# Performance work log

Measured on AMD Instinct MI355X. Metric: run time of the kernel, lower is better.

The kernel has to match this reference:

```python
import jax, jax.numpy as jnp
import numpy as np

KERNEL = 5
DILATIONS = (3, 1)
N_HEADS = 8
LN_EPS = 1e-5


def unfold1d(x, kernel, dilation, pad):
    # x: (N, H, S) -> (N, H, S, kernel) dilated sliding windows (same length)
    xp = jnp.pad(x, ((0, 0), (0, 0), (pad, pad)))
    S = x.shape[-1]
    idx = jnp.arange(S)[:, None] + jnp.arange(kernel)[None, :] * dilation  # (S, K)
    return xp[:, :, idx]  # (N, H, S, K)


def dilated_mha(q, k, v, Ws, bs, Wo, bo):
    # q,k,v: (B, S, D); Ws: (2, split, split); Wo: (D, D)
    B, S, D = q.shape
    ndil = len(DILATIONS)
    hpd = N_HEADS // ndil            # heads per dilation
    dk = D // N_HEADS
    split = D // ndil
    scale = dk ** (-0.5)
    outs, probs = [], []
    for i, dil in enumerate(DILATIONS):
        pad = dil * (KERNEL - 1) // 2
        sl = slice(i * split, (i + 1) * split)
        qi = q[..., sl] @ Ws[i].T + bs[i]
        ki = k[..., sl] @ Ws[i].T + bs[i]
        vi = v[..., sl] @ Ws[i].T + bs[i]
        # (B,S,hpd,dk) -> (B,dk,hpd,S), matching torch transpose(1,2).permute(0,3,1,2)
        to4 = lambda x: jnp.transpose(x.reshape(B, S, hpd, dk), (0, 3, 2, 1))
        qi4, ki4, vi4 = to4(qi), to4(ki), to4(vi)
        # unfold then reinterpret (B*dk,hpd,...) as (B*hpd,dk,...) exactly as torch .reshape does
        kp = unfold1d(ki4.reshape(B * dk, hpd, S), KERNEL, dil, pad).reshape(B * hpd, dk, S, KERNEL)
        vp = unfold1d(vi4.reshape(B * dk, hpd, S), KERNEL, dil, pad).reshape(B * hpd, dk, S, KERNEL)
        qr = qi4.reshape(B * hpd, dk, S)
        scores = jnp.einsum('nds,ndsk->nsk', qr, kp) * scale   # (B*hpd, S, K)
        p = jax.nn.softmax(scores, axis=-1)
        out = jnp.einsum('nsk,ndsk->nds', p, vp)               # (B*hpd, dk, S)
        out = jnp.transpose(out.reshape(B, hpd, dk, S), (0, 3, 1, 2)).reshape(B, S, split)
        outs.append(out)
        probs.append(p.reshape(B, hpd, S, KERNEL))
    o = jnp.concatenate(outs, axis=-1) @ Wo.T + bo
    return o, jnp.concatenate(probs, axis=1)


def layer_norm(x, g, b):
    mu = jnp.mean(x, axis=-1, keepdims=True)
    var = jnp.mean((x - mu) ** 2, axis=-1, keepdims=True)
    return (x - mu) * jax.lax.rsqrt(var + LN_EPS) * g + b


def setup_inputs() -> dict:
    key = jax.random.key(0)
    ks = jax.random.split(key, 6)
    B, S, D = 32, 2048, 256
    split = D // 2
    q_emb = jax.random.normal(ks[0], (B, S, D), dtype=jnp.float32)
    s_emb = jax.random.normal(ks[1], (B, S, D), dtype=jnp.float32)
    lens = jax.random.randint(ks[2], (B,), 5, S, dtype=jnp.int32)
    W_lin = jax.random.normal(ks[3], (3, 2, split, split), dtype=jnp.float32) * (split ** -0.5)
    b_lin = jnp.zeros((3, 2, split), dtype=jnp.float32)
    W_out = jax.random.normal(ks[4], (3, D, D), dtype=jnp.float32) * (D ** -0.5)
    b_out = jnp.zeros((3, D), dtype=jnp.float32)
    ln_g = jnp.ones((3, D), dtype=jnp.float32)
    ln_b = jnp.zeros((3, D), dtype=jnp.float32)
    return {"q_emb": q_emb, "s_emb": s_emb, "lens": lens, "W_lin": W_lin,
            "b_lin": b_lin, "W_out": W_out, "b_out": b_out, "ln_g": ln_g, "ln_b": ln_b}


def reference(q_emb, s_emb, lens, W_lin, b_lin, W_out, b_out, ln_g, ln_b):
    # CASTransformer.forward, shortcut=True path, eval mode (dropout=id, mask unused)
    a1, _ = dilated_mha(q_emb, q_emb, q_emb, W_lin[0], b_lin[0], W_out[0], b_out[0])
    hq = layer_norm(q_emb + a1, ln_g[0], ln_b[0])
    a2, q_scores = dilated_mha(s_emb, s_emb, s_emb, W_lin[1], b_lin[1], W_out[1], b_out[1])
    hs = layer_norm(s_emb + a2, ln_g[1], ln_b[1])
    a3, _ = dilated_mha(hq, hq, hs, W_lin[2], b_lin[2], W_out[2], b_out[2])
    z = layer_norm(hq + a3, ln_g[2], ln_b[2])
    return z, q_scores
```

## Files before the change

### kernel.cpp

```cpp
#include <hip/hip_runtime.h>
#include <hip/hip_bf16.h>

typedef __bf16 bf16x8 __attribute__((ext_vector_type(8)));
typedef float  f32x4  __attribute__((ext_vector_type(4)));
typedef unsigned int u32;
typedef u32 u32x4 __attribute__((ext_vector_type(4)));
typedef unsigned short ushort_t;

__device__ inline float bf2f(ushort_t h) {
    union { u32 u; float f; } v; v.u = ((u32)h) << 16; return v.f;
}
__device__ inline ushort_t f2bf(float f) {
    union { float f; u32 u; } v; v.f = f;
    u32 u = v.u;
    return (ushort_t)((u + 0x7fffu + ((u >> 16) & 1u)) >> 16);
}
__device__ inline bf16x8 load_bf8(const ushort_t* p) {
    u32x4 u = *reinterpret_cast<const u32x4*>(p);
    return __builtin_bit_cast(bf16x8, u);
}
__device__ inline bf16x8 load8_in(const void* base, size_t idx, int f32flag) {
    if (!f32flag) return load_bf8((const ushort_t*)base + idx);
    const float* pf = (const float*)base + idx;
    f32x4 a = *reinterpret_cast<const f32x4*>(pf);
    f32x4 b = *reinterpret_cast<const f32x4*>(pf + 4);
    bf16x8 r;
#pragma unroll
    for (int j = 0; j < 4; ++j) { r[j] = (__bf16)a[j]; r[4 + j] = (__bf16)b[j]; }
    return r;
}
__device__ inline float ld_in(const void* base, size_t idx, int f32flag) {
    return f32flag ? ((const float*)base)[idx] : bf2f(((const ushort_t*)base)[idx]);
}

#define XT_STRIDE 264

__global__ __launch_bounds__(256) void detect_kernel(const u32* __restrict__ d, int n,
                                                     int* __restrict__ flag) {
    const int t = threadIdx.x;
    int cn = 0, co = 0;
    for (int i = t; i < n; i += 256) {
        const u32 w = d[i];
        const u32 e  = (w >> 7) & 0xFF;
        const u32 fe = (w >> 23) & 0xFF;
        cn += (e >= 100 && e <= 135) ? 1 : 0;
        co += (((w & 0xFFFFu) == 0u) && fe >= 100 && fe <= 140) ? 1 : 0;
    }
    __shared__ int sn[256], so[256];
    sn[t] = cn; so[t] = co; __syncthreads();
    for (int o = 128; o; o >>= 1) {
        if (t < o) { sn[t] += sn[t + o]; so[t] += so[t + o]; }
        __syncthreads();
    }
    if (t == 0) {
        const int CN = sn[0], CO = so[0];
        const int is_f32 = (2 * CN < n) && ((2 * CO > n) || (20 * CN > n));
        *flag = is_f32 ? 1 : 0;
    }
}

__device__ inline int f_of(const int* flags, int i) { return i < 0 ? 0 : flags[i]; }
__device__ inline int out_f32(const int* flags) {
    return flags[0] | flags[1] | flags[3] | flags[4] | flags[5] | flags[6] | flags[7] | flags[8];
}

__global__ __launch_bounds__(256) void proj_kernel(
    const void* __restrict__ X, int xi,
    const void* __restrict__ W, size_t lw,
    const void* __restrict__ Bv, size_t lb,
    ushort_t* __restrict__ Y, const int* __restrict__ flags)
{
    const int xf = f_of(flags, xi);
    const int wf = flags[3], bf = flags[4];
    const int tid  = threadIdx.x;
    const int wave = tid >> 6, lane = tid & 63;
    const int dil  = wave >> 1;
    const int n_off = (wave & 1) * 64;
    const int m0   = blockIdx.x * 64;
    const int l15  = lane & 15, quad = lane >> 4;

    f32x4 acc[4][4] = {};
    for (int kc = 0; kc < 4; ++kc) {
        bf16x8 a[4], b[4];
#pragma unroll
        for (int mt = 0; mt < 4; ++mt)
            a[mt] = load8_in(X, (size_t)(m0 + mt * 16 + l15) * 256 + dil * 128 + kc * 32 + quad * 8, xf);
#pragma unroll
        for (int nt = 0; nt < 4; ++nt)
            b[nt] = load8_in(W, lw + (size_t)dil * 16384 + (size_t)(n_off + nt * 16 + l15) * 128 + kc * 32 + quad * 8, wf);
#pragma unroll
        for (int mt = 0; mt < 4; ++mt)
#pragma unroll
            for (int nt = 0; nt < 4; ++nt)
                acc[mt][nt] = __builtin_amdgcn_mfma_f32_16x16x32_bf16(a[mt], b[nt], acc[mt][nt], 0, 0, 0);
    }
#pragma unroll
    for (int mt = 0; mt < 4; ++mt) {
#pragma unroll
        for (int nt = 0; nt < 4; ++nt) {
            const int ncol = n_off + nt * 16 + l15;
            const float bias = ld_in(Bv, lb + dil * 128 + ncol, bf);
#pragma unroll
            for (int r = 0; r < 4; ++r) {
                const int row = m0 + mt * 16 + quad * 4 + r;
                Y[(size_t)row * 256 + dil * 128 + ncol] = f2bf(acc[mt][nt][r] + bias);
            }
        }
    }
}

__global__ __launch_bounds__(256) void proj_inplace_kernel(
    ushort_t* __restrict__ X,
    const void* __restrict__ W, size_t lw,
    const void* __restrict__ Bv, size_t lb,
    const int* __restrict__ flags)
{
    __shared__ ushort_t xt[64 * XT_STRIDE];
    const int wf = flags[3], bf = flags[4];
    const int tid = threadIdx.x;
    const int m0  = blockIdx.x * 64;
#pragma unroll
    for (int i = 0; i < 8; ++i) {
        const int chunk = tid + 256 * i;
        const int row = chunk >> 5, cc = chunk & 31;
        *reinterpret_cast<u32x4*>(&xt[row * XT_STRIDE + cc * 8]) =
            *reinterpret_cast<const u32x4*>(X + (size_t)(m0 + row) * 256 + cc * 8);
    }
    __syncthreads();

    const int wave = tid >> 6, lane = tid & 63;
    const int dil  = wave >> 1;
    const int n_off = (wave & 1) * 64;
    const int l15  = lane & 15, quad = lane >> 4;

    f32x4 acc[4][4] = {};
    for (int kc = 0; kc < 4; ++kc) {
        bf16x8 a[4], b[4];
#pragma unroll
        for (int mt = 0; mt < 4; ++mt)
            a[mt] = load_bf8(&xt[(mt * 16 + l15) * XT_STRIDE + dil * 128 + kc * 32 + quad * 8]);
#pragma unroll
        for (int nt = 0; nt < 4; ++nt)
            b[nt] = load8_in(W, lw + (size_t)dil * 16384 + (size_t)(n_off + nt * 16 + l15) * 128 + kc * 32 + quad * 8, wf);
#pragma unroll
        for (int mt = 0; mt < 4; ++mt)
#pragma unroll
            for (int nt = 0; nt < 4; ++nt)
                acc[mt][nt] = __builtin_amdgcn_mfma_f32_16x16x32_bf16(a[mt], b[nt], acc[mt][nt], 0, 0, 0);
    }
#pragma unroll
    for (int mt = 0; mt < 4; ++mt) {
#pragma unroll
        for (int nt = 0; nt < 4; ++nt) {
            const int ncol = n_off + nt * 16 + l15;
            const float bias = ld_in(Bv, lb + dil * 128 + ncol, bf);
#pragma unroll
            for (int r = 0; r < 4; ++r) {
                const int row = m0 + mt * 16 + quad * 4 + r;
                X[(size_t)row * 256 + dil * 128 + ncol] = f2bf(acc[mt][nt][r] + bias);
            }
        }
    }
}

__global__ __launch_bounds__(256) void fused_attn_oln_kernel(
    const ushort_t* __restrict__ P, const ushort_t* __restrict__ V,
    const void* __restrict__ R, int ri,
    const void* __restrict__ W, size_t lw,
    const void* __restrict__ Bv, size_t lb,
    const void* __restrict__ G, const void* __restrict__ Bt, size_t lg,
    void* __restrict__ H, int h_out,
    void* __restrict__ probs_base,
    const int* __restrict__ flags)
{
    __shared__ ushort_t xt[64 * XT_STRIDE];
    __shared__ float lsum[4][64], lsq[4][64];

    const int wf = flags[5], bvf = flags[6], gf = flags[7], btf = flags[8];
    const int rf = f_of(flags, ri);
    const int og = out_f32(flags);
    const int of = h_out ? og : 0;

    const int tid = threadIdx.x;
    const int m0  = blockIdx.x * 64;
    const int bb  = m0 >> 11;
    const int s0  = m0 & 2047;
    const size_t rowbase = (size_t)bb * 2048;
    const float scale = 0.17677669529663687f;

#pragma unroll
    for (int it = 0; it < 2; ++it) {
        const int task = tid + 256 * it;
        const int r  = task & 63;
        const int dg = task >> 6;
        const int dil = dg >> 2, g = dg & 3;
        const int dila = dil ? 1 : 3;
        const int s = s0 + r;
        const size_t chan0 = (size_t)dil * 128 + g * 8;

        const ushort_t* qr = P + (rowbase + s) * 256 + chan0;
        float qv[4][8];
#pragma unroll
        for (int h = 0; h < 4; ++h) {
            bf16x8 t = load_bf8(qr + h * 32);
#pragma unroll
            for (int j = 0; j < 8; ++j) qv[h][j] = (float)t[j];
        }
        float sc[5];
#pragma unroll
        for (int kk = 0; kk < 5; ++kk) {
            const int sp = s + (kk - 2) * dila;
            float a = 0.f;
            if (sp >= 0 && sp < 2048) {
                const ushort_t* kr = P + (rowbase + sp) * 256 + chan0;
#pragma unroll
                for (int h = 0; h < 4; ++h) {
                    bf16x8 t = load_bf8(kr + h * 32);
#pragma unroll
                    for (int j = 0; j < 8; ++j) a += qv[h][j] * (float)t[j];
                }
                a *= scale;
            }
            sc[kk] = a;
        }
        float mx = sc[0];
#pragma unroll
        for (int kk = 1; kk < 5; ++kk) mx = fmaxf(mx, sc[kk]);
        float p[5], sum = 0.f;
#pragma unroll
        for (int kk = 0; kk < 5; ++kk) { p[kk] = __expf(sc[kk] - mx); sum += p[kk]; }
        const float inv = 1.f / sum;
#pragma unroll
        for (int kk = 0; kk < 5; ++kk) p[kk] *= inv;

        float o[4][8] = {};
#pragma unroll
        for (int kk = 0; kk < 5; ++kk) {
            const int sp = s + (kk - 2) * dila;
            if (sp < 0 || sp >= 2048) continue;
            const ushort_t* vr = V + (rowbase + sp) * 256 + chan0;
#pragma unroll
            for (int h = 0; h < 4; ++h) {
                bf16x8 t = load_bf8(vr + h * 32);
#pragma unroll
                for (int j = 0; j < 8; ++j) o[h][j] += p[kk] * (float)t[j];
            }
        }
        ushort_t* op = &xt[r * XT_STRIDE + dil * 128 + g * 32];
#pragma unroll
        for (int c = 0; c < 4; ++c) {
            u32x4 w;
#pragma unroll
            for (int t4 = 0; t4 < 4; ++t4) {
                const int d2a = c * 8 + t4 * 2, d2b = d2a + 1;
                const u32 lo = f2bf(o[d2a & 3][d2a >> 2]);
                const u32 hi = f2bf(o[d2b & 3][d2b >> 2]);
                w[t4] = lo | (hi << 16);
            }
            *reinterpret_cast<u32x4*>(op + c * 8) = w;
        }
        if (probs_base != nullptr) {
            const size_t pb = 16777216 + ((size_t)((bb * 8 + dg) * 2048 + s)) * 5;
            if (og) {
                float* pp = (float*)probs_base;
#pragma unroll
                for (int kk = 0; kk < 5; ++kk) pp[pb + kk] = p[kk];
            } else {
                ushort_t* pp = (ushort_t*)probs_base;
#pragma unroll
                for (int kk = 0; kk < 5; ++kk) pp[pb + kk] = f2bf(p[kk]);
            }
        }
    }
    __syncthreads();

    const int wave = tid >> 6, lane = tid & 63;
    const int n_off = wave * 64;
    const int l15 = lane & 15, quad = lane >> 4;

    f32x4 acc[4][4] = {};
    for (int kc = 0; kc < 8; ++kc) {
        bf16x8 a[4], b[4];
#pragma unroll
        for (int mt = 0; mt < 4; ++mt)
            a[mt] = load_bf8(&xt[(mt * 16 + l15) * XT_STRIDE + kc * 32 + quad * 8]);
#pragma unroll
        for (int nt = 0; nt < 4; ++nt)
            b[nt] = load8_in(W, lw + (size_t)(n_off + nt * 16 + l15) * 256 + kc * 32 + quad * 8, wf);
#pragma unroll
        for (int mt = 0; mt < 4; ++mt)
#pragma unroll
            for (int nt = 0; nt < 4; ++nt)
                acc[mt][nt] = __builtin_amdgcn_mfma_f32_16x16x32_bf16(a[mt], b[nt], acc[mt][nt], 0, 0, 0);
    }

    float bias[4];
#pragma unroll
    for (int nt = 0; nt < 4; ++nt) bias[nt] = ld_in(Bv, lb + n_off + nt * 16 + l15, bvf);

    float psum[4][4] = {}, psq[4][4] = {};
#pragma unroll
    for (int mt = 0; mt < 4; ++mt) {
#pragma unroll
        for (int rr = 0; rr < 4; ++rr) {
            const size_t rrow = (size_t)(m0 + mt * 16 + quad * 4 + rr) * 256 + l15;
#pragma unroll
            for (int nt = 0; nt < 4; ++nt) {
                float v = acc[mt][nt][rr] + bias[nt] + ld_in(R, rrow + n_off + nt * 16, rf);
                acc[mt][nt][rr] = v;
                psum[mt][rr] += v;
                psq[mt][rr]  += v * v;
            }
        }
    }
#pragma unroll
    for (int off = 1; off <= 8; off <<= 1) {
#pragma unroll
        for (int mt = 0; mt < 4; ++mt)
#pragma unroll
            for (int rr = 0; rr < 4; ++rr) {
                psum[mt][rr] += __shfl_xor(psum[mt][rr], off);
                psq[mt][rr]  += __shfl_xor(psq[mt][rr],  off);
            }
    }
    if (l15 == 0) {
#pragma unroll
        for (int mt = 0; mt < 4; ++mt)
#pragma unroll
            for (int rr = 0; rr < 4; ++rr) {
                const int row = mt * 16 + quad * 4 + rr;
                lsum[wave][row] = psum[mt][rr];
                lsq[wave][row]  = psq[mt][rr];
            }
    }
    __syncthreads();

    float gl[4], bl[4];
#pragma unroll
    for (int nt = 0; nt < 4; ++nt) {
        gl[nt] = ld_in(G,  lg + n_off + nt * 16 + l15, gf);
        bl[nt] = ld_in(Bt, lg + n_off + nt * 16 + l15, btf);
    }
#pragma unroll
    for (int mt = 0; mt < 4; ++mt) {
#pragma unroll
        for (int rr = 0; rr < 4; ++rr) {
            const int row = mt * 16 + quad * 4 + rr;
            const float sm = lsum[0][row] + lsum[1][row] + lsum[2][row] + lsum[3][row];
            const float q2 = lsq[0][row]  + lsq[1][row]  + lsq[2][row]  + lsq[3][row];
            const float mu  = sm * (1.f / 256.f);
            const float var = q2 * (1.f / 256.f) - mu * mu;
            const float rs  = rsqrtf(var + 1e-5f);
            const size_t hrow = (size_t)(m0 + row) * 256 + l15;
#pragma unroll
            for (int nt = 0; nt < 4; ++nt) {
                const float hv = (acc[mt][nt][rr] - mu) * rs * gl[nt] + bl[nt];
                if (of) ((float*)H)[hrow + n_off + nt * 16] = hv;
                else    ((ushort_t*)H)[hrow + n_off + nt * 16] = f2bf(hv);
            }
        }
    }
}

extern "C" void kernel_launch(void* const* d_in, const int* in_sizes, int n_in,
                              void* d_out, int out_size, void* d_ws, size_t ws_size,
                              hipStream_t stream) {
    const void* q_emb = d_in[0];
    const void* s_emb = d_in[1];
    const void* W_lin = d_in[3];
    const void* b_lin = d_in[4];
    const void* W_out = d_in[5];
    const void* b_out = d_in[6];
    const void* ln_g  = d_in[7];
    const void* ln_b  = d_in[8];

    const size_t SLOT = 16777216;
    int*      flags = (int*)d_ws;
    ushort_t* SA = (ushort_t*)((char*)d_ws + 256);
    ushort_t* SB = SA + SLOT;
    ushort_t* SC = SA + 2 * SLOT;

    const dim3 blk(256);
    detect_kernel<<<1, blk, 0, stream>>>((const u32*)q_emb, 16384, flags + 0);
    detect_kernel<<<1, blk, 0, stream>>>((const u32*)s_emb, 16384, flags + 1);
    detect_kernel<<<1, blk, 0, stream>>>((const u32*)W_lin, 16384, flags + 3);
    detect_kernel<<<1, blk, 0, stream>>>((const u32*)b_lin,   384, flags + 4);
    detect_kernel<<<1, blk, 0, stream>>>((const u32*)W_out, 16384, flags + 5);
    detect_kernel<<<1, blk, 0, stream>>>((const u32*)b_out,   384, flags + 6);
    detect_kernel<<<1, blk, 0, stream>>>((const u32*)ln_g,    384, flags + 7);
    detect_kernel<<<1, blk, 0, stream>>>((const u32*)ln_b,    384, flags + 8);

    proj_kernel<<<1024, blk, 0, stream>>>(q_emb, 0, W_lin, 0, b_lin, 0, SC, flags);
    fused_attn_oln_kernel<<<1024, blk, 0, stream>>>(SC, SC, q_emb, 0,
        W_out, 0, b_out, 0, ln_g, ln_b, 0, SA, 0, nullptr, flags);
    proj_kernel<<<1024, blk, 0, stream>>>(s_emb, 1, W_lin, 32768, b_lin, 256, SC, flags);
    fused_attn_oln_kernel<<<1024, blk, 0, stream>>>(SC, SC, s_emb, 1,
        W_out, 65536, b_out, 256, ln_g, ln_b, 256, SB, 0, d_out, flags);
    proj_kernel<<<1024, blk, 0, stream>>>(SA, -1, W_lin, 65536, b_lin, 512, SC, flags);
    proj_inplace_kernel<<<1024, blk, 0, stream>>>(SB, W_lin, 65536, b_lin, 512, flags);
    fused_attn_oln_kernel<<<1024, blk, 0, stream>>>(SC, SB, SA, -1,
        W_out, 131072, b_out, 512, ln_g, ln_b, 512, d_out, 1, nullptr, flags);
}
```

Baseline: 697.8 us.

## Fuse input projections and next-stage projections into per-stage mega kernels

Merges the eight detect launches into one multi-block kernel. Folds each stage's QKV projection into the attention kernel: projected rows for the block plus an 8-row halo on each side go into LDS, so attention reads from shared memory rather than a global intermediate. The LayerNorm output is also projected right away with the third-stage weights, which removes the separate proj and in-place proj launches. This cuts launches and global round trips for intermediates, at the cost of recomputing the halo rows, more LDS per block (possible occupancy loss), and weights held in registers.

```diff
diff --git a/kernel.cpp b/kernel.cpp
--- a/kernel.cpp
+++ b/kernel.cpp
@@ -33,14 +33,35 @@
     return f32flag ? ((const float*)base)[idx] : bf2f(((const ushort_t*)base)[idx]);
 }
 
-#define XT_STRIDE 264
-
-__global__ __launch_bounds__(256) void detect_kernel(const u32* __restrict__ d, int n,
-                                                     int* __restrict__ flag) {
+__device__ inline int f_of(const int* flags, int i) { return i < 0 ? 0 : flags[i]; }
+__device__ inline int out_f32(const int* flags) {
+    return flags[0] | flags[1] | flags[3] | flags[4] | flags[5] | flags[6] | flags[7] | flags[8];
+}
+
+#define PT_ROWS   80
+#define PT_STRIDE 266
+#define XT_STRIDE 266
+
+__global__ __launch_bounds__(256) void detect8_kernel(
+    const u32* p0, int n0, const u32* p1, int n1, const u32* p2, int n2, const u32* p3, int n3,
+    const u32* p4, int n4, const u32* p5, int n5, const u32* p6, int n6, const u32* p7, int n7,
+    int* __restrict__ flags)
+{
+    const u32* p; int n, slot;
+    switch (blockIdx.x) {
+        case 0: p = p0; n = n0; slot = 0; break;
+        case 1: p = p1; n = n1; slot = 1; break;
+        case 2: p = p2; n = n2; slot = 3; break;
+        case 3: p = p3; n = n3; slot = 4; break;
+        case 4: p = p4; n = n4; slot = 5; break;
+        case 5: p = p5; n = n5; slot = 6; break;
+        case 6: p = p6; n = n6; slot = 7; break;
+        default: p = p7; n = n7; slot = 8; break;
+    }
     const int t = threadIdx.x;
     int cn = 0, co = 0;
     for (int i = t; i < n; i += 256) {
-        const u32 w = d[i];
+        const u32 w = p[i];
         const u32 e  = (w >> 7) & 0xFF;
         const u32 fe = (w >> 23) & 0xFF;
         cn += (e >= 100 && e <= 135) ? 1 : 0;
@@ -54,155 +75,108 @@
     }
     if (t == 0) {
         const int CN = sn[0], CO = so[0];
-        const int is_f32 = (2 * CN < n) && ((2 * CO > n) || (20 * CN > n));
-        *flag = is_f32 ? 1 : 0;
-    }
-}
-
-__device__ inline int f_of(const int* flags, int i) { return i < 0 ? 0 : flags[i]; }
-__device__ inline int out_f32(const int* flags) {
-    return flags[0] | flags[1] | flags[3] | flags[4] | flags[5] | flags[6] | flags[7] | flags[8];
-}
-
-__global__ __launch_bounds__(256) void proj_kernel(
+        flags[slot] = ((2 * CN < n) && ((2 * CO > n) || (20 * CN > n))) ? 1 : 0;
+    }
+}
+
+template<int STAGE>
+__global__ __launch_bounds__(256) void mega_kernel(
     const void* __restrict__ X, int xi,
-    const void* __restrict__ W, size_t lw,
-    const void* __restrict__ Bv, size_t lb,
-    ushort_t* __restrict__ Y, const int* __restrict__ flags)
-{
-    const int xf = f_of(flags, xi);
-    const int wf = flags[3], bf = flags[4];
-    const int tid  = threadIdx.x;
-    const int wave = tid >> 6, lane = tid & 63;
-    const int dil  = wave >> 1;
-    const int n_off = (wave & 1) * 64;
-    const int m0   = blockIdx.x * 64;
-    const int l15  = lane & 15, quad = lane >> 4;
-
-    f32x4 acc[4][4] = {};
-    for (int kc = 0; kc < 4; ++kc) {
-        bf16x8 a[4], b[4];
-#pragma unroll
-        for (int mt = 0; mt < 4; ++mt)
-            a[mt] = load8_in(X, (size_t)(m0 + mt * 16 + l15) * 256 + dil * 128 + kc * 32 + quad * 8, xf);
-#pragma unroll
-        for (int nt = 0; nt < 4; ++nt)
-            b[nt] = load8_in(W, lw + (size_t)dil * 16384 + (size_t)(n_off + nt * 16 + l15) * 128 + kc * 32 + quad * 8, wf);
-#pragma unroll
-        for (int mt = 0; mt < 4; ++mt)
-#pragma unroll
-            for (int nt = 0; nt < 4; ++nt)
-                acc[mt][nt] = __builtin_amdgcn_mfma_f32_16x16x32_bf16(a[mt], b[nt], acc[mt][nt], 0, 0, 0);
-    }
-#pragma unroll
-    for (int mt = 0; mt < 4; ++mt) {
-#pragma unroll
-        for (int nt = 0; nt < 4; ++nt) {
-            const int ncol = n_off + nt * 16 + l15;
-            const float bias = ld_in(Bv, lb + dil * 128 + ncol, bf);
-#pragma unroll
-            for (int r = 0; r < 4; ++r) {
-                const int row = m0 + mt * 16 + quad * 4 + r;
-                Y[(size_t)row * 256 + dil * 128 + ncol] = f2bf(acc[mt][nt][r] + bias);
-            }
-        }
-    }
-}
-
-__global__ __launch_bounds__(256) void proj_inplace_kernel(
-    ushort_t* __restrict__ X,
-    const void* __restrict__ W, size_t lw,
-    const void* __restrict__ Bv, size_t lb,
-    const int* __restrict__ flags)
-{
-    __shared__ ushort_t xt[64 * XT_STRIDE];
-    const int wf = flags[3], bf = flags[4];
-    const int tid = threadIdx.x;
-    const int m0  = blockIdx.x * 64;
-#pragma unroll
-    for (int i = 0; i < 8; ++i) {
-        const int chunk = tid + 256 * i;
-        const int row = chunk >> 5, cc = chunk & 31;
-        *reinterpret_cast<u32x4*>(&xt[row * XT_STRIDE + cc * 8]) =
-            *reinterpret_cast<const u32x4*>(X + (size_t)(m0 + row) * 256 + cc * 8);
-    }
-    __syncthreads();
-
-    const int wave = tid >> 6, lane = tid & 63;
-    const int dil  = wave >> 1;
-    const int n_off = (wave & 1) * 64;
-    const int l15  = lane & 15, quad = lane >> 4;
-
-    f32x4 acc[4][4] = {};
-    for (int kc = 0; kc < 4; ++kc) {
-        bf16x8 a[4], b[4];
-#pragma unroll
-        for (int mt = 0; mt < 4; ++mt)
-            a[mt] = load_bf8(&xt[(mt * 16 + l15) * XT_STRIDE + dil * 128 + kc * 32 + quad * 8]);
-#pragma unroll
-        for (int nt = 0; nt < 4; ++nt)
-            b[nt] = load8_in(W, lw + (size_t)dil * 16384 + (size_t)(n_off + nt * 16 + l15) * 128 + kc * 32 + quad * 8, wf);
-#pragma unroll
-        for (int mt = 0; mt < 4; ++mt)
-#pragma unroll
-            for (int nt = 0; nt < 4; ++nt)
-                acc[mt][nt] = __builtin_amdgcn_mfma_f32_16x16x32_bf16(a[mt], b[nt], acc[mt][nt], 0, 0, 0);
-    }
-#pragma unroll
-    for (int mt = 0; mt < 4; ++mt) {
-#pragma unroll
-        for (int nt = 0; nt < 4; ++nt) {
-            const int ncol = n_off + nt * 16 + l15;
-            const float bias = ld_in(Bv, lb + dil * 128 + ncol, bf);
-#pragma unroll
-            for (int r = 0; r < 4; ++r) {
-                const int row = m0 + mt * 16 + quad * 4 + r;
-                X[(size_t)row * 256 + dil * 128 + ncol] = f2bf(acc[mt][nt][r] + bias);
-            }
-        }
-    }
-}
-
-__global__ __launch_bounds__(256) void fused_attn_oln_kernel(
-    const ushort_t* __restrict__ P, const ushort_t* __restrict__ V,
-    const void* __restrict__ R, int ri,
-    const void* __restrict__ W, size_t lw,
-    const void* __restrict__ Bv, size_t lb,
+    const ushort_t* __restrict__ PRE,
+    const ushort_t* __restrict__ VSRC,
+    const void* __restrict__ Wl,  size_t lwl,
+    const void* __restrict__ bl,  size_t lbl,
+    const void* __restrict__ WlC, size_t lwlC,
+    const void* __restrict__ blC, size_t lblC,
+    const void* __restrict__ Wo,  size_t lwo,
+    const void* __restrict__ bo,  size_t lbo,
+    const void* __restrict__ R,   int ri,
     const void* __restrict__ G, const void* __restrict__ Bt, size_t lg,
-    void* __restrict__ H, int h_out,
+    ushort_t* __restrict__ HA,
+    ushort_t* __restrict__ PC,
+    void* __restrict__ Z,
     void* __restrict__ probs_base,
     const int* __restrict__ flags)
 {
+    __shared__ ushort_t Pt[PT_ROWS * PT_STRIDE];
     __shared__ ushort_t xt[64 * XT_STRIDE];
     __shared__ float lsum[4][64], lsq[4][64];
 
-    const int wf = flags[5], bvf = flags[6], gf = flags[7], btf = flags[8];
-    const int rf = f_of(flags, ri);
+    const int tid  = threadIdx.x;
+    const int wave = tid >> 6, lane = tid & 63;
+    const int l15  = lane & 15, quad = lane >> 4;
+    const int m0   = blockIdx.x * 64;
+    const int bb   = m0 >> 11;
+    const int s0   = m0 & 2047;
+    const size_t rowbase = (size_t)bb * 2048;
     const int og = out_f32(flags);
-    const int of = h_out ? og : 0;
-
-    const int tid = threadIdx.x;
-    const int m0  = blockIdx.x * 64;
-    const int bb  = m0 >> 11;
-    const int s0  = m0 & 2047;
-    const size_t rowbase = (size_t)bb * 2048;
+
+    if (STAGE < 2) {
+        const int xf = f_of(flags, xi);
+        const int wf = flags[3], bff = flags[4];
+        const int dil = wave >> 1;
+        const int no  = (wave & 1) * 64;
+        bf16x8 bfr[4][4];
+#pragma unroll
+        for (int kc = 0; kc < 4; ++kc)
+#pragma unroll
+            for (int nt = 0; nt < 4; ++nt)
+                bfr[kc][nt] = load8_in(Wl, lwl + (size_t)dil * 16384 +
+                    (size_t)(no + nt * 16 + l15) * 128 + kc * 32 + quad * 8, wf);
+        float bias[4];
+#pragma unroll
+        for (int nt = 0; nt < 4; ++nt)
+            bias[nt] = ld_in(bl, lbl + dil * 128 + no + nt * 16 + l15, bff);
+
+#pragma unroll
+        for (int mt = 0; mt < 5; ++mt) {
+            int srow = s0 - 8 + mt * 16 + l15;
+            srow = srow < 0 ? 0 : (srow > 2047 ? 2047 : srow);
+            const size_t abase = (rowbase + srow) * 256 + dil * 128 + quad * 8;
+            f32x4 acc[4] = {};
+#pragma unroll
+            for (int kc = 0; kc < 4; ++kc) {
+                bf16x8 a = load8_in(X, abase + kc * 32, xf);
+#pragma unroll
+                for (int nt = 0; nt < 4; ++nt)
+                    acc[nt] = __builtin_amdgcn_mfma_f32_16x16x32_bf16(a, bfr[kc][nt], acc[nt], 0, 0, 0);
+            }
+#pragma unroll
+            for (int nt = 0; nt < 4; ++nt) {
+                const int ncol = dil * 128 + no + nt * 16 + l15;
+#pragma unroll
+                for (int r = 0; r < 4; ++r)
+                    Pt[(mt * 16 + quad * 4 + r) * PT_STRIDE + ncol] = f2bf(acc[nt][r] + bias[nt]);
+            }
+        }
+    } else {
+#pragma unroll
+        for (int i = 0; i < 10; ++i) {
+            const int chunk = tid + 256 * i;
+            const int trow = chunk >> 5, cc = chunk & 31;
+            int srow = s0 - 8 + trow;
+            srow = srow < 0 ? 0 : (srow > 2047 ? 2047 : srow);
+            *reinterpret_cast<u32x4*>(&Pt[trow * PT_STRIDE + cc * 8]) =
+                *reinterpret_cast<const u32x4*>(PRE + (rowbase + srow) * 256 + cc * 8);
+        }
+    }
+    __syncthreads();
+
     const float scale = 0.17677669529663687f;
-
 #pragma unroll
     for (int it = 0; it < 2; ++it) {
         const int task = tid + 256 * it;
-        const int r  = task & 63;
-        const int dg = task >> 6;
+        const int r = task & 63, dg = task >> 6;
         const int dil = dg >> 2, g = dg & 3;
         const int dila = dil ? 1 : 3;
         const int s = s0 + r;
-        const size_t chan0 = (size_t)dil * 128 + g * 8;
-
-        const ushort_t* qr = P + (rowbase + s) * 256 + chan0;
+        const int ch = dil * 128 + g * 8;
+
+        const ushort_t* qp = &Pt[(r + 8) * PT_STRIDE + ch];
         float qv[4][8];
 #pragma unroll
         for (int h = 0; h < 4; ++h) {
-            bf16x8 t = load_bf8(qr + h * 32);
+            bf16x8 t = load_bf8(qp + h * 32);
 #pragma unroll
             for (int j = 0; j < 8; ++j) qv[h][j] = (float)t[j];
         }
@@ -212,10 +186,10 @@
             const int sp = s + (kk - 2) * dila;
             float a = 0.f;
             if (sp >= 0 && sp < 2048) {
-                const ushort_t* kr = P + (rowbase + sp) * 256 + chan0;
+                const ushort_t* kp = &Pt[(r + 8 + (kk - 2) * dila) * PT_STRIDE + ch];
 #pragma unroll
                 for (int h = 0; h < 4; ++h) {
-                    bf16x8 t = load_bf8(kr + h * 32);
+                    bf16x8 t = load_bf8(kp + h * 32);
 #pragma unroll
                     for (int j = 0; j < 8; ++j) a += qv[h][j] * (float)t[j];
                 }
@@ -238,10 +212,12 @@
         for (int kk = 0; kk < 5; ++kk) {
             const int sp = s + (kk - 2) * dila;
             if (sp < 0 || sp >= 2048) continue;
-            const ushort_t* vr = V + (rowbase + sp) * 256 + chan0;
+            const ushort_t* vp = (STAGE < 2)
+                ? &Pt[(r + 8 + (kk - 2) * dila) * PT_STRIDE + ch]
+                : (VSRC + (rowbase + sp) * 256 + ch);
 #pragma unroll
             for (int h = 0; h < 4; ++h) {
-                bf16x8 t = load_bf8(vr + h * 32);
+                bf16x8 t = load_bf8(vp + h * 32);
 #pragma unroll
                 for (int j = 0; j < 8; ++j) o[h][j] += p[kk] * (float)t[j];
             }
@@ -259,7 +235,7 @@
             }
             *reinterpret_cast<u32x4*>(op + c * 8) = w;
         }
-        if (probs_base != nullptr) {
+        if (STAGE == 1) {
             const size_t pb = 16777216 + ((size_t)((bb * 8 + dg) * 2048 + s)) * 5;
             if (og) {
                 float* pp = (float*)probs_base;
@@ -274,9 +250,9 @@
     }
     __syncthreads();
 
-    const int wave = tid >> 6, lane = tid & 63;
+    const int wf2 = flags[5], bvf = flags[6], gf = flags[7], btf = flags[8];
+    const int rf = f_of(flags, ri);
     const int n_off = wave * 64;
-    const int l15 = lane & 15, quad = lane >> 4;
 
     f32x4 acc[4][4] = {};
     for (int kc = 0; kc < 8; ++kc) {
@@ -286,7 +262,7 @@
             a[mt] = load_bf8(&xt[(mt * 16 + l15) * XT_STRIDE + kc * 32 + quad * 8]);
 #pragma unroll
         for (int nt = 0; nt < 4; ++nt)
-            b[nt] = load8_in(W, lw + (size_t)(n_off + nt * 16 + l15) * 256 + kc * 32 + quad * 8, wf);
+            b[nt] = load8_in(Wo, lwo + (size_t)(n_off + nt * 16 + l15) * 256 + kc * 32 + quad * 8, wf2);
 #pragma unroll
         for (int mt = 0; mt < 4; ++mt)
 #pragma unroll
@@ -296,7 +272,7 @@
 
     float bias[4];
 #pragma unroll
-    for (int nt = 0; nt < 4; ++nt) bias[nt] = ld_in(Bv, lb + n_off + nt * 16 + l15, bvf);
+    for (int nt = 0; nt < 4; ++nt) bias[nt] = ld_in(bo, lbo + n_off + nt * 16 + l15, bvf);
 
     float psum[4][4] = {}, psq[4][4] = {};
 #pragma unroll
@@ -335,11 +311,11 @@
     }
     __syncthreads();
 
-    float gl[4], bl[4];
+    float gl[4], blv[4];
 #pragma unroll
     for (int nt = 0; nt < 4; ++nt) {
-        gl[nt] = ld_in(G,  lg + n_off + nt * 16 + l15, gf);
-        bl[nt] = ld_in(Bt, lg + n_off + nt * 16 + l15, btf);
+        gl[nt]  = ld_in(G,  lg + n_off + nt * 16 + l15, gf);
+        blv[nt] = ld_in(Bt, lg + n_off + nt * 16 + l15, btf);
     }
 #pragma unroll
     for (int mt = 0; mt < 4; ++mt) {
@@ -351,12 +327,56 @@
             const float mu  = sm * (1.f / 256.f);
             const float var = q2 * (1.f / 256.f) - mu * mu;
             const float rs  = rsqrtf(var + 1e-5f);
-            const size_t hrow = (size_t)(m0 + row) * 256 + l15;
 #pragma unroll
             for (int nt = 0; nt < 4; ++nt) {
-                const float hv = (acc[mt][nt][rr] - mu) * rs * gl[nt] + bl[nt];
-                if (of) ((float*)H)[hrow + n_off + nt * 16] = hv;
-                else    ((ushort_t*)H)[hrow + n_off + nt * 16] = f2bf(hv);
+                const int col = n_off + nt * 16 + l15;
+                const float hv = (acc[mt][nt][rr] - mu) * rs * gl[nt] + blv[nt];
+                if (STAGE == 0) {
+                    HA[(size_t)(m0 + row) * 256 + col] = f2bf(hv);
+                    xt[row * XT_STRIDE + col] = f2bf(hv);
+                } else if (STAGE == 1) {
+                    xt[row * XT_STRIDE + col] = f2bf(hv);
+                } else {
+                    const size_t zi = (size_t)(m0 + row) * 256 + col;
+                    if (og) ((float*)Z)[zi] = hv;
+                    else    ((ushort_t*)Z)[zi] = f2bf(hv);
+                }
+            }
+        }
+    }
+
+    if (STAGE < 2) {
+        __syncthreads();
+        const int wf = flags[3], bff = flags[4];
+        const int dil = wave >> 1;
+        const int no  = (wave & 1) * 64;
+        bf16x8 bfr[4][4];
+#pragma unroll
+        for (int kc = 0; kc < 4; ++kc)
+#pragma unroll
+            for (int nt = 0; nt < 4; ++nt)
+                bfr[kc][nt] = load8_in(WlC, lwlC + (size_t)dil * 16384 +
+                    (size_t)(no + nt * 16 + l15) * 128 + kc * 32 + quad * 8, wf);
+        float bias2[4];
+#pragma unroll
+        for (int nt = 0; nt < 4; ++nt)
+            bias2[nt] = ld_in(blC, lblC + dil * 128 + no + nt * 16 + l15, bff);
+#pragma unroll
+        for (int mt = 0; mt < 4; ++mt) {
+            f32x4 acc2[4] = {};
+#pragma unroll
+            for (int kc = 0; kc < 4; ++kc) {
+                bf16x8 a = load_bf8(&xt[(mt * 16 + l15) * XT_STRIDE + dil * 128 + kc * 32 + quad * 8]);
+#pragma unroll
+                for (int nt = 0; nt < 4; ++nt)
+                    acc2[nt] = __builtin_amdgcn_mfma_f32_16x16x32_bf16(a, bfr[kc][nt], acc2[nt], 0, 0, 0);
+            }
+#pragma unroll
+            for (int nt = 0; nt < 4; ++nt) {
+                const int ncol = dil * 128 + no + nt * 16 + l15;
+#pragma unroll
+                for (int r = 0; r < 4; ++r)
+                    PC[(size_t)(m0 + mt * 16 + quad * 4 + r) * 256 + ncol] = f2bf(acc2[nt][r] + bias2[nt]);
             }
         }
     }
@@ -380,24 +400,34 @@
     ushort_t* SB = SA + SLOT;
     ushort_t* SC = SA + 2 * SLOT;
 
-    const dim3 blk(256);
-    detect_kernel<<<1, blk, 0, stream>>>((const u32*)q_emb, 16384, flags + 0);
-    detect_kernel<<<1, blk, 0, stream>>>((const u32*)s_emb, 16384, flags + 1);
-    detect_kernel<<<1, blk, 0, stream>>>((const u32*)W_lin, 16384, flags + 3);
-    detect_kernel<<<1, blk, 0, stream>>>((const u32*)b_lin,   384, flags + 4);
-    detect_kernel<<<1, blk, 0, stream>>>((const u32*)W_out, 16384, flags + 5);
-    detect_kernel<<<1, blk, 0, stream>>>((const u32*)b_out,   384, flags + 6);
-    detect_kernel<<<1, blk, 0, stream>>>((const u32*)ln_g,    384, flags + 7);
-    detect_kernel<<<1, blk, 0, stream>>>((const u32*)ln_b,    384, flags + 8);
-
-    proj_kernel<<<1024, blk, 0, stream>>>(q_emb, 0, W_lin, 0, b_lin, 0, SC, flags);
-    fused_attn_oln_kernel<<<1024, blk, 0, stream>>>(SC, SC, q_emb, 0,
-        W_out, 0, b_out, 0, ln_g, ln_b, 0, SA, 0, nullptr, flags);
-    proj_kernel<<<1024, blk, 0, stream>>>(s_emb, 1, W_lin, 32768, b_lin, 256, SC, flags);
-    fused_attn_oln_kernel<<<1024, blk, 0, stream>>>(SC, SC, s_emb, 1,
-        W_out, 65536, b_out, 256, ln_g, ln_b, 256, SB, 0, d_out, flags);
-    proj_kernel<<<1024, blk, 0, stream>>>(SA, -1, W_lin, 65536, b_lin, 512, SC, flags);
-    proj_inplace_kernel<<<1024, blk, 0, stream>>>(SB, W_lin, 65536, b_lin, 512, flags);
-    fused_attn_oln_kernel<<<1024, blk, 0, stream>>>(SC, SB, SA, -1,
-        W_out, 131072, b_out, 512, ln_g, ln_b, 512, d_out, 1, nullptr, flags);
-}
+    detect8_kernel<<<8, 256, 0, stream>>>(
+        (const u32*)q_emb, 16384, (const u32*)s_emb, 16384,
+        (const u32*)W_lin, 16384, (const u32*)b_lin, 384,
+        (const u32*)W_out, 16384, (const u32*)b_out, 384,
+        (const u32*)ln_g, 384, (const u32*)ln_b, 384, flags);
+
+    mega_kernel<0><<<1024, 256, 0, stream>>>(
+        q_emb, 0, nullptr, nullptr,
+        W_lin, 0, b_lin, 0,
+        W_lin, 65536, b_lin, 512,
+        W_out, 0, b_out, 0,
+        q_emb, 0,
+        ln_g, ln_b, 0,
+        SA, SC, nullptr, nullptr, flags);
+    mega_kernel<1><<<1024, 256, 0, stream>>>(
+        s_emb, 1, nullptr, nullptr,
+        W_lin, 32768, b_lin, 256,
+        W_lin, 65536, b_lin, 512,
+        W_out, 65536, b_out, 256,
+        s_emb, 1,
+        ln_g, ln_b, 256,
+        nullptr, SB, nullptr, d_out, flags);
+    mega_kernel<2><<<1024, 256, 0, stream>>>(
+        nullptr, -1, SC, SB,
+        nullptr, 0, nullptr, 0,
+        nullptr, 0, nullptr, 0,
+        W_out, 131072, b_out, 512,
+        SA, -1,
+        ln_g, ln_b, 512,
+        nullptr, nullptr, d_out, nullptr, flags);
+}
```

Measured after the change: 732.7 us. +5.0%, slower.
